# Optimization experiments

Hardware: AMD Instinct MI355X
Metric: run time of the kernel (lower is better)

The kernel has to match this reference:

```python
import jax, jax.numpy as jnp
import numpy as np

N, C, A, CI = 32768, 512, 64, 1024  # n_locations, content_size, address_size, controller_input_size
EPS = 1e-7


def setup_inputs() -> dict:
    key = jax.random.key(0)
    ks = jax.random.split(key, 12)
    g = lambda i, shape, s=1.0: jax.random.normal(ks[i], shape, dtype=jnp.float32) * s
    xav = lambda i, shape: g(i, shape, float(np.sqrt(2.0 / (shape[0] + shape[1]))))
    return {
        "controller_hidden_state": g(0, (N, 1)),
        "controller_input": g(1, (CI, 1)),
        "memory_contents": g(2, (N, C), 0.5),
        "memory_addresses": xav(3, (N, A)),
        "exp_mov_avg_similarity": g(4, (N, 1), 0.1),
        "W_query": xav(5, (C + A, N)),
        "b_query": jnp.zeros((C + A, 1), jnp.float32),
        "u_sharpen": xav(6, (1, N)),
        "b_sharpen": jnp.zeros((1,), jnp.float32),
        "u_lru": xav(7, (1, N)),
        "b_lru": jnp.zeros((1,), jnp.float32),
        "W_erase": xav(8, (C, N)),
        "b_erase": jnp.zeros((C, 1), jnp.float32),
        "W_content_hidden": xav(9, (C, N)),
        "W_content_input": xav(10, (C, CI)),
        "u_content_alpha": xav(11, (N + CI, 1)),
        "b_content_alpha": jnp.zeros((1, 1), jnp.float32),
    }


def reference(controller_hidden_state, controller_input, memory_contents, memory_addresses,
              exp_mov_avg_similarity, W_query, b_query, u_sharpen, b_sharpen, u_lru, b_lru,
              W_erase, b_erase, W_content_hidden, W_content_input, u_content_alpha,
              b_content_alpha):
    h, x = controller_hidden_state, controller_input
    # ---- address_memory ----
    full_mem = jnp.concatenate([memory_addresses, memory_contents], axis=1)  # [N, A+C]
    query = W_query @ h + b_query                                            # [A+C, 1]
    beta = jax.nn.softplus(u_sharpen @ h + b_sharpen) + 1.0                  # [1, 1]
    q = query[:, 0]
    q_norm = jnp.maximum(jnp.linalg.norm(q), EPS)
    m_norm = jnp.maximum(jnp.linalg.norm(full_mem, axis=1), EPS)             # [N]
    cos = (full_mem @ q) / (m_norm * q_norm)                                 # [N] cosine sim per location
    sim = (beta[0, 0] * cos)[:, None]                                        # [N, 1]
    gamma = jax.nn.sigmoid(u_lru @ h + b_lru)                                # [1, 1] LRU gate
    addr = jax.nn.softmax(sim - gamma * exp_mov_avg_similarity, axis=0)      # [N, 1]
    # (state buffer update, next-step only): new_ema = 0.1*ema + 0.9*sim
    # ---- update (vectorized erase/write over all N locations) ----
    erase = W_erase @ h + b_erase                                            # [C, 1]
    alpha = u_content_alpha.T @ jnp.concatenate([h, x], axis=0) + b_content_alpha  # [1, 1]
    cand = jax.nn.relu(W_content_hidden @ h + alpha * (W_content_input @ x))       # [C, 1]
    new_mem = (1.0 - addr * erase.T) * memory_contents + addr * cand.T       # [N, C]
    # ---- read (on updated memory) ----
    new_full = jnp.concatenate([memory_addresses, new_mem], axis=1)          # [N, A+C]
    read = new_full.T @ addr                                                 # [A+C, 1]
    return read
```

## Files before the change

kernel.cpp:

```cpp
#include <hip/hip_runtime.h>
#include <hip/hip_bf16.h>
#include <math.h>

#define NN 32768
#define CC 512
#define AA 64
#define CIN 1024
#define EPSV 1e-7f


#define QOFF 2128
#define SOFF 2704
#define PMOFF 35472
#define PAOFF 559760

__global__ __launch_bounds__(256) void k1_gemv(
    const float* __restrict__ h, const float* __restrict__ x,
    const float* __restrict__ Wq, const float* __restrict__ Wer,
    const float* __restrict__ Wch, const float* __restrict__ Wci,
    const float* __restrict__ ush, const float* __restrict__ ulr,
    const float* __restrict__ uca, float* __restrict__ ws)
{
    const int b = blockIdx.x, tid = threadIdx.x;
    const int wave = tid >> 6, lane = tid & 63;
    __shared__ float hs[4096];
    __shared__ float red[4][8];

    if (b < 1600) {
        const int rg = b >> 3, chunk = b & 7;
        const float4* h4 = reinterpret_cast<const float4*>(h) + chunk * 1024;
        float4* hs4 = reinterpret_cast<float4*>(hs);
        #pragma unroll
        for (int k = 0; k < 4; ++k) hs4[k * 256 + tid] = h4[k * 256 + tid];
        __syncthreads();
        const int r0 = rg * 8;
        const float* mat; int base;
        if (r0 < 576)       { mat = Wq;  base = 0; }
        else if (r0 < 1088) { mat = Wer; base = 576; }
        else                { mat = Wch; base = 1088; }
        const float4* m4 = reinterpret_cast<const float4*>(
            mat + (size_t)(r0 - base) * NN + chunk * 4096);
        const int rs = NN / 4;
        float acc[8] = {0,0,0,0,0,0,0,0};
        #pragma unroll
        for (int it = 0; it < 4; ++it) {
            float4 hb = hs4[it * 256 + tid];
            #pragma unroll
            for (int r = 0; r < 8; ++r) {
                float4 a = m4[(size_t)r * rs + it * 256 + tid];
                acc[r] += a.x * hb.x + a.y * hb.y + a.z * hb.z + a.w * hb.w;
            }
        }
        #pragma unroll
        for (int r = 0; r < 8; ++r) {
            #pragma unroll
            for (int off = 32; off >= 1; off >>= 1)
                acc[r] += __shfl_xor(acc[r], off);
        }
        if (lane == 0) {
            #pragma unroll
            for (int r = 0; r < 8; ++r) red[wave][r] = acc[r];
        }
        __syncthreads();
        if (tid < 8) {
            float v = red[0][tid] + red[1][tid] + red[2][tid] + red[3][tid];
            atomicAdd(ws + r0 + tid, v);
        }
    } else if (b < 1664) {
        const int rg = b - 1600;
        float4 xv = reinterpret_cast<const float4*>(x)[tid];
        const float4* m4 = reinterpret_cast<const float4*>(
            Wci + (size_t)rg * 8 * CIN);
        float acc[8];
        #pragma unroll
        for (int r = 0; r < 8; ++r) {
            float4 a = m4[r * 256 + tid];
            acc[r] = a.x * xv.x + a.y * xv.y + a.z * xv.z + a.w * xv.w;
        }
        #pragma unroll
        for (int r = 0; r < 8; ++r) {
            #pragma unroll
            for (int off = 32; off >= 1; off >>= 1)
                acc[r] += __shfl_xor(acc[r], off);
        }
        if (lane == 0) {
            #pragma unroll
            for (int r = 0; r < 8; ++r) red[wave][r] = acc[r];
        }
        __syncthreads();
        if (tid < 8) {
            float v = red[0][tid] + red[1][tid] + red[2][tid] + red[3][tid];
            ws[1600 + rg * 8 + tid] = v;
        }
    } else {
        const int t = b - 1664, sd = t >> 3, chunk = t & 7;
        const float* vec = (sd == 0) ? ush : (sd == 1) ? ulr : uca;
        const float4* v4 = reinterpret_cast<const float4*>(vec) + chunk * 1024;
        const float4* h4 = reinterpret_cast<const float4*>(h) + chunk * 1024;
        float acc = 0.f;
        #pragma unroll
        for (int it = 0; it < 4; ++it) {
            float4 a = v4[it * 256 + tid];
            float4 hb = h4[it * 256 + tid];
            acc += a.x * hb.x + a.y * hb.y + a.z * hb.z + a.w * hb.w;
        }
        if (sd == 2 && chunk == 0) {
            float4 a = reinterpret_cast<const float4*>(uca)[NN / 4 + tid];
            float4 xv = reinterpret_cast<const float4*>(x)[tid];
            acc += a.x * xv.x + a.y * xv.y + a.z * xv.z + a.w * xv.w;
        }
        #pragma unroll
        for (int off = 32; off >= 1; off >>= 1)
            acc += __shfl_xor(acc, off);
        if (lane == 0) red[wave][0] = acc;
        __syncthreads();
        if (tid == 0)
            atomicAdd(ws + 2112 + sd,
                      red[0][0] + red[1][0] + red[2][0] + red[3][0]);
    }
}

__global__ __launch_bounds__(256) void k1b_scalars(
    const float* __restrict__ bq, const float* __restrict__ bsh,
    const float* __restrict__ blr, const float* __restrict__ bca,
    float* __restrict__ ws)
{
    __shared__ float red[256];
    const int tid = threadIdx.x;
    float s = 0.f;
    for (int j = tid; j < 576; j += 256) {
        float q = ws[j] + bq[j];
        ws[QOFF + j] = q;
        s += q * q;
    }
    red[tid] = s; __syncthreads();
    for (int st = 128; st > 0; st >>= 1) {
        if (tid < st) red[tid] += red[tid + st];
        __syncthreads();
    }
    if (tid == 0) {
        float qn = fmaxf(sqrtf(red[0]), EPSV);
        float bp = ws[2112] + bsh[0];
        float beta = (bp > 20.f ? bp : log1pf(expf(bp))) + 1.0f;
        float gp = ws[2113] + blr[0];
        float gamma = 1.f / (1.f + expf(-gp));
        float alpha = ws[2114] + bca[0];
        ws[2112] = beta; ws[2113] = gamma; ws[2114] = alpha; ws[2115] = qn;
    }
}

__global__ __launch_bounds__(256) void k2_sim(
    const float* __restrict__ Mm, const float* __restrict__ Ad,
    const float* __restrict__ ema, const float* __restrict__ ws,
    float* __restrict__ ws_s)
{
    const int tid = threadIdx.x, wave = tid >> 6, lane = tid & 63;
    const float beta = ws[2112], gamma = ws[2113], qn = ws[2115];
    const float ql = ws[QOFF + lane];
    float4 qa = *reinterpret_cast<const float4*>(ws + QOFF + 64 + lane * 8);
    float4 qb = *reinterpret_cast<const float4*>(ws + QOFF + 68 + lane * 8);
    float qm[8] = {qa.x, qa.y, qa.z, qa.w, qb.x, qb.y, qb.z, qb.w};
    #pragma unroll
    for (int j = 0; j < 4; ++j) {
        const int i = blockIdx.x * 16 + wave * 4 + j;
        float a = Ad[(size_t)i * AA + lane];
        float4 m0 = *reinterpret_cast<const float4*>(Mm + (size_t)i * CC + lane * 8);
        float4 m1 = *reinterpret_cast<const float4*>(Mm + (size_t)i * CC + lane * 8 + 4);
        float mm[8] = {m0.x, m0.y, m0.z, m0.w, m1.x, m1.y, m1.z, m1.w};
        float dot = a * ql, nn = a * a;
        #pragma unroll
        for (int k = 0; k < 8; ++k) { float f = mm[k]; dot += f * qm[k]; nn += f * f; }
        #pragma unroll
        for (int off = 32; off >= 1; off >>= 1) {
            dot += __shfl_xor(dot, off);
            nn  += __shfl_xor(nn, off);
        }
        if (lane == 0) {
            float mn = fmaxf(sqrtf(nn), EPSV);
            ws_s[i] = beta * (dot / (mn * qn)) - gamma * ema[i];
        }
    }
}

__global__ __launch_bounds__(1024) void k3_softmax(float* __restrict__ ws)
{
    const float* s = ws + SOFF;
    __shared__ float lmx[16], lz[16], ls2[16], bc[1];
    const int tid = threadIdx.x, lane = tid & 63, wid = tid >> 6;
    float v[32];
    float mx = -1e30f;
    #pragma unroll
    for (int j = 0; j < 32; ++j) { v[j] = s[tid + 1024 * j]; mx = fmaxf(mx, v[j]); }
    #pragma unroll
    for (int off = 32; off >= 1; off >>= 1) mx = fmaxf(mx, __shfl_xor(mx, off));
    if (lane == 0) lmx[wid] = mx;
    __syncthreads();
    if (tid == 0) { float m = lmx[0]; for (int k = 1; k < 16; ++k) m = fmaxf(m, lmx[k]); bc[0] = m; }
    __syncthreads();
    mx = bc[0];
    float z = 0.f, s2 = 0.f;
    #pragma unroll
    for (int j = 0; j < 32; ++j) { float e = expf(v[j] - mx); z += e; s2 += e * e; }
    #pragma unroll
    for (int off = 32; off >= 1; off >>= 1) { z += __shfl_xor(z, off); s2 += __shfl_xor(s2, off); }
    if (lane == 0) { lz[wid] = z; ls2[wid] = s2; }
    __syncthreads();
    if (tid == 0) {
        float Z = 0.f, S = 0.f;
        for (int k = 0; k < 16; ++k) { Z += lz[k]; S += ls2[k]; }
        ws[2116] = mx; ws[2117] = 1.f / Z; ws[2118] = S / (Z * Z);
    }
}

__global__ __launch_bounds__(256) void k4_acc(
    const float* __restrict__ Mm, const float* __restrict__ Ad,
    const float* __restrict__ ws, float* __restrict__ pm, float* __restrict__ pa)
{
    __shared__ float lds[4][1024];
    const int b = blockIdx.x, tid = threadIdx.x, wave = tid >> 6, lane = tid & 63;
    const float* s = ws + SOFF;
    const float mx = ws[2116], invZ = ws[2117];
    if (b < 512) {
        float a1[8] = {0,0,0,0,0,0,0,0};
        float a2[8] = {0,0,0,0,0,0,0,0};
        for (int j = 0; j < 16; ++j) {
            const int i = b * 64 + j * 4 + wave;
            float w1 = expf(s[i] - mx) * invZ;
            float w2 = w1 * w1;
            float4 m0 = *reinterpret_cast<const float4*>(Mm + (size_t)i * CC + lane * 8);
            float4 m1 = *reinterpret_cast<const float4*>(Mm + (size_t)i * CC + lane * 8 + 4);
            float mm[8] = {m0.x, m0.y, m0.z, m0.w, m1.x, m1.y, m1.z, m1.w};
            #pragma unroll
            for (int k = 0; k < 8; ++k) { float f = mm[k]; a1[k] += w1 * f; a2[k] += w2 * f; }
        }
        #pragma unroll
        for (int k = 0; k < 8; ++k) {
            lds[wave][lane * 8 + k] = a1[k];
            lds[wave][512 + lane * 8 + k] = a2[k];
        }
        __syncthreads();
        for (int e = tid; e < 1024; e += 256) {
            float v = lds[0][e] + lds[1][e] + lds[2][e] + lds[3][e];
            pm[(size_t)e * 512 + b] = v;
        }
    } else {
        const int bb = b - 512;
        float acc = 0.f;
        for (int j = 0; j < 64; ++j) {
            const int i = bb * 256 + j * 4 + wave;
            float w1 = expf(s[i] - mx) * invZ;
            acc += w1 * Ad[(size_t)i * AA + lane];
        }
        lds[wave][lane] = acc;
        __syncthreads();
        if (tid < 64) {
            float v = lds[0][tid] + lds[1][tid] + lds[2][tid] + lds[3][tid];
            pa[tid * 128 + bb] = v;
        }
    }
}

__global__ __launch_bounds__(256) void k5_final(
    const float* __restrict__ ws, const float* __restrict__ pm,
    const float* __restrict__ pa, const float* __restrict__ ber,
    float* __restrict__ out)
{
    __shared__ float red[256];
    const int b = blockIdx.x, tid = threadIdx.x;
    if (b < 64) {
        float v = (tid < 128) ? pa[b * 128 + tid] : 0.f;
        red[tid] = v; __syncthreads();
        for (int st = 128; st > 0; st >>= 1) {
            if (tid < st) red[tid] += red[tid + st];
            __syncthreads();
        }
        if (tid == 0) out[b] = red[0];
    } else {
        const int c = b - 64;
        float v1 = pm[(size_t)c * 512 + tid] + pm[(size_t)c * 512 + tid + 256];
        float v2 = pm[(size_t)(512 + c) * 512 + tid] + pm[(size_t)(512 + c) * 512 + tid + 256];
        red[tid] = v1; __syncthreads();
        for (int st = 128; st > 0; st >>= 1) {
            if (tid < st) red[tid] += red[tid + st];
            __syncthreads();
        }
        float s1 = red[0];
        __syncthreads();
        red[tid] = v2; __syncthreads();
        for (int st = 128; st > 0; st >>= 1) {
            if (tid < st) red[tid] += red[tid + st];
            __syncthreads();
        }
        if (tid == 0) {
            float s2v = red[0];
            float er = ws[576 + c] + ber[c];
            float ch = ws[1088 + c], cx = ws[1600 + c];
            float alpha = ws[2114], S2 = ws[2118];
            float cand = fmaxf(ch + alpha * cx, 0.f);
            out[64 + c] = s1 - er * s2v + S2 * cand;
        }
    }
}

extern "C" void kernel_launch(void* const* d_in, const int* in_sizes, int n_in,
                              void* d_out, int out_size, void* d_ws, size_t ws_size,
                              hipStream_t stream)
{
    const float* h   = (const float*)d_in[0];
    const float* x   = (const float*)d_in[1];
    const float* Mm  = (const float*)d_in[2];
    const float* Ad  = (const float*)d_in[3];
    const float* ema = (const float*)d_in[4];
    const float* Wq  = (const float*)d_in[5];
    const float* bq  = (const float*)d_in[6];
    const float* ush = (const float*)d_in[7];
    const float* bsh = (const float*)d_in[8];
    const float* ulr = (const float*)d_in[9];
    const float* blr = (const float*)d_in[10];
    const float* Wer = (const float*)d_in[11];
    const float* ber = (const float*)d_in[12];
    const float* Wch = (const float*)d_in[13];
    const float* Wci = (const float*)d_in[14];
    const float* uca = (const float*)d_in[15];
    const float* bca = (const float*)d_in[16];

    float* ws   = (float*)d_ws;
    float* ws_s = ws + SOFF;
    float* pm   = ws + PMOFF;
    float* pa   = ws + PAOFF;
    float* out  = (float*)d_out;

    hipMemsetAsync(ws, 0, QOFF * sizeof(float), stream);

    hipLaunchKernelGGL(k1_gemv,    dim3(1688), dim3(256),  0, stream,
                       h, x, Wq, Wer, Wch, Wci, ush, ulr, uca, ws);
    hipLaunchKernelGGL(k1b_scalars, dim3(1),   dim3(256),  0, stream,
                       bq, bsh, blr, bca, ws);
    hipLaunchKernelGGL(k2_sim,     dim3(2048), dim3(256),  0, stream, Mm, Ad, ema, ws, ws_s);
    hipLaunchKernelGGL(k3_softmax, dim3(1),    dim3(1024), 0, stream, ws);
    hipLaunchKernelGGL(k4_acc,     dim3(640),  dim3(256),  0, stream, Mm, Ad, ws, pm, pa);
    hipLaunchKernelGGL(k5_final,   dim3(576),  dim3(256),  0, stream, ws, pm, pa, ber, out);
}
```

Baseline: 330.2 us.

## Fuse similarity, softmax and weighted accumulation into one pass with online softmax

Merges the similarity, global softmax and weighted-accumulation kernels into a single pass over memory using a per-wave online (running-max) softmax. Each block writes partial sums plus local max, Z and S2 statistics, and a small kernel rescales them into per-block coefficients that the final kernel applies. This removes the second full read of the 64 MB memory matrix and one launch. The GEMV weights are now loaded with nontemporal loads and software prefetch. The cost is extra exp and rescale work per row, fewer blocks in the fused kernel, and slightly different floating-point rounding.

```diff
diff --git a/kernel.cpp b/kernel.cpp
--- a/kernel.cpp
+++ b/kernel.cpp
@@ -10,9 +10,20 @@
 
 
 #define QOFF 2128
-#define SOFF 2704
-#define PMOFF 35472
-#define PAOFF 559760
+#define STOFF 2704
+#define SCOFF 4240
+#define PAOFF 5264
+#define PMOFF 38032
+
+typedef float floatx4 __attribute__((ext_vector_type(4)));
+
+__device__ __forceinline__ float4 ntload4(const float4* p) {
+    floatx4 v = __builtin_nontemporal_load(reinterpret_cast<const floatx4*>(p));
+    return make_float4(v.x, v.y, v.z, v.w);
+}
+__device__ __forceinline__ float ntloadf(const float* p) {
+    return __builtin_nontemporal_load(p);
+}
 
 __global__ __launch_bounds__(256) void k1_gemv(
     const float* __restrict__ h, const float* __restrict__ x,
@@ -42,13 +53,25 @@
             mat + (size_t)(r0 - base) * NN + chunk * 4096);
         const int rs = NN / 4;
         float acc[8] = {0,0,0,0,0,0,0,0};
+        float4 cur[8];
+        #pragma unroll
+        for (int r = 0; r < 8; ++r) cur[r] = ntload4(m4 + (size_t)r * rs + tid);
         #pragma unroll
         for (int it = 0; it < 4; ++it) {
+            float4 nxt[8];
+            if (it < 3) {
+                #pragma unroll
+                for (int r = 0; r < 8; ++r)
+                    nxt[r] = ntload4(m4 + (size_t)r * rs + (it + 1) * 256 + tid);
+            }
             float4 hb = hs4[it * 256 + tid];
             #pragma unroll
-            for (int r = 0; r < 8; ++r) {
-                float4 a = m4[(size_t)r * rs + it * 256 + tid];
-                acc[r] += a.x * hb.x + a.y * hb.y + a.z * hb.z + a.w * hb.w;
+            for (int r = 0; r < 8; ++r)
+                acc[r] += cur[r].x * hb.x + cur[r].y * hb.y +
+                          cur[r].z * hb.z + cur[r].w * hb.w;
+            if (it < 3) {
+                #pragma unroll
+                for (int r = 0; r < 8; ++r) cur[r] = nxt[r];
             }
         }
         #pragma unroll
@@ -74,7 +97,7 @@
         float acc[8];
         #pragma unroll
         for (int r = 0; r < 8; ++r) {
-            float4 a = m4[r * 256 + tid];
+            float4 a = ntload4(m4 + r * 256 + tid);
             acc[r] = a.x * xv.x + a.y * xv.y + a.z * xv.z + a.w * xv.w;
         }
         #pragma unroll
@@ -149,23 +172,28 @@
     }
 }
 
-__global__ __launch_bounds__(256) void k2_sim(
+__global__ __launch_bounds__(512) void k2f_fused(
     const float* __restrict__ Mm, const float* __restrict__ Ad,
     const float* __restrict__ ema, const float* __restrict__ ws,
-    float* __restrict__ ws_s)
-{
-    const int tid = threadIdx.x, wave = tid >> 6, lane = tid & 63;
+    float* __restrict__ pm, float* __restrict__ pa, float* __restrict__ stats)
+{
+    __shared__ float lw[8][1092];
+    const int b = blockIdx.x, tid = threadIdx.x, wave = tid >> 6, lane = tid & 63;
     const float beta = ws[2112], gamma = ws[2113], qn = ws[2115];
     const float ql = ws[QOFF + lane];
     float4 qa = *reinterpret_cast<const float4*>(ws + QOFF + 64 + lane * 8);
     float4 qb = *reinterpret_cast<const float4*>(ws + QOFF + 68 + lane * 8);
     float qm[8] = {qa.x, qa.y, qa.z, qa.w, qb.x, qb.y, qb.z, qb.w};
-    #pragma unroll
-    for (int j = 0; j < 4; ++j) {
-        const int i = blockIdx.x * 16 + wave * 4 + j;
-        float a = Ad[(size_t)i * AA + lane];
-        float4 m0 = *reinterpret_cast<const float4*>(Mm + (size_t)i * CC + lane * 8);
-        float4 m1 = *reinterpret_cast<const float4*>(Mm + (size_t)i * CC + lane * 8 + 4);
+
+    float a1[8] = {0,0,0,0,0,0,0,0};
+    float a2[8] = {0,0,0,0,0,0,0,0};
+    float aA = 0.f, m_run = -1e30f, Z = 0.f, S2 = 0.f;
+    const int base = b * 64 + wave * 8;
+    for (int j = 0; j < 8; ++j) {
+        const int i = base + j;
+        float a = ntloadf(Ad + (size_t)i * AA + lane);
+        float4 m0 = ntload4(reinterpret_cast<const float4*>(Mm + (size_t)i * CC + lane * 8));
+        float4 m1 = ntload4(reinterpret_cast<const float4*>(Mm + (size_t)i * CC + lane * 8 + 4));
         float mm[8] = {m0.x, m0.y, m0.z, m0.w, m1.x, m1.y, m1.z, m1.w};
         float dot = a * ql, nn = a * a;
         #pragma unroll
@@ -175,100 +203,105 @@
             dot += __shfl_xor(dot, off);
             nn  += __shfl_xor(nn, off);
         }
-        if (lane == 0) {
-            float mn = fmaxf(sqrtf(nn), EPSV);
-            ws_s[i] = beta * (dot / (mn * qn)) - gamma * ema[i];
-        }
-    }
-}
-
-__global__ __launch_bounds__(1024) void k3_softmax(float* __restrict__ ws)
-{
-    const float* s = ws + SOFF;
-    __shared__ float lmx[16], lz[16], ls2[16], bc[1];
-    const int tid = threadIdx.x, lane = tid & 63, wid = tid >> 6;
-    float v[32];
-    float mx = -1e30f;
+        float mn = fmaxf(sqrtf(nn), EPSV);
+        float s = beta * (dot / (mn * qn)) - gamma * ema[i];
+        if (s > m_run) {
+            float f = expf(m_run - s);
+            float f2 = f * f;
+            Z *= f; S2 *= f2; aA *= f;
+            #pragma unroll
+            for (int k = 0; k < 8; ++k) { a1[k] *= f; a2[k] *= f2; }
+            m_run = s;
+        }
+        float w = expf(s - m_run);
+        float w2 = w * w;
+        Z += w; S2 += w2; aA += w * a;
+        #pragma unroll
+        for (int k = 0; k < 8; ++k) { a1[k] += w * mm[k]; a2[k] += w2 * mm[k]; }
+    }
     #pragma unroll
-    for (int j = 0; j < 32; ++j) { v[j] = s[tid + 1024 * j]; mx = fmaxf(mx, v[j]); }
+    for (int k = 0; k < 8; ++k) {
+        lw[wave][lane * 8 + k] = a1[k];
+        lw[wave][512 + lane * 8 + k] = a2[k];
+    }
+    lw[wave][1024 + lane] = aA;
+    if (lane == 0) { lw[wave][1088] = m_run; lw[wave][1089] = Z; lw[wave][1090] = S2; }
+    __syncthreads();
+    float mb = lw[0][1088];
     #pragma unroll
-    for (int off = 32; off >= 1; off >>= 1) mx = fmaxf(mx, __shfl_xor(mx, off));
-    if (lane == 0) lmx[wid] = mx;
-    __syncthreads();
-    if (tid == 0) { float m = lmx[0]; for (int k = 1; k < 16; ++k) m = fmaxf(m, lmx[k]); bc[0] = m; }
-    __syncthreads();
-    mx = bc[0];
-    float z = 0.f, s2 = 0.f;
+    for (int w = 1; w < 8; ++w) mb = fmaxf(mb, lw[w][1088]);
+    float fw[8];
     #pragma unroll
-    for (int j = 0; j < 32; ++j) { float e = expf(v[j] - mx); z += e; s2 += e * e; }
-    #pragma unroll
-    for (int off = 32; off >= 1; off >>= 1) { z += __shfl_xor(z, off); s2 += __shfl_xor(s2, off); }
-    if (lane == 0) { lz[wid] = z; ls2[wid] = s2; }
-    __syncthreads();
+    for (int w = 0; w < 8; ++w) fw[w] = expf(lw[w][1088] - mb);
+    for (int e = tid; e < 1024; e += 512) {
+        float v = 0.f;
+        if (e < 512) {
+            #pragma unroll
+            for (int w = 0; w < 8; ++w) v += fw[w] * lw[w][e];
+        } else {
+            #pragma unroll
+            for (int w = 0; w < 8; ++w) v += fw[w] * fw[w] * lw[w][e];
+        }
+        pm[(size_t)e * 512 + b] = v;
+    }
+    if (tid < 64) {
+        float v = 0.f;
+        #pragma unroll
+        for (int w = 0; w < 8; ++w) v += fw[w] * lw[w][1024 + tid];
+        pa[tid * 512 + b] = v;
+    }
     if (tid == 0) {
-        float Z = 0.f, S = 0.f;
-        for (int k = 0; k < 16; ++k) { Z += lz[k]; S += ls2[k]; }
-        ws[2116] = mx; ws[2117] = 1.f / Z; ws[2118] = S / (Z * Z);
-    }
-}
-
-__global__ __launch_bounds__(256) void k4_acc(
-    const float* __restrict__ Mm, const float* __restrict__ Ad,
-    const float* __restrict__ ws, float* __restrict__ pm, float* __restrict__ pa)
-{
-    __shared__ float lds[4][1024];
-    const int b = blockIdx.x, tid = threadIdx.x, wave = tid >> 6, lane = tid & 63;
-    const float* s = ws + SOFF;
-    const float mx = ws[2116], invZ = ws[2117];
-    if (b < 512) {
-        float a1[8] = {0,0,0,0,0,0,0,0};
-        float a2[8] = {0,0,0,0,0,0,0,0};
-        for (int j = 0; j < 16; ++j) {
-            const int i = b * 64 + j * 4 + wave;
-            float w1 = expf(s[i] - mx) * invZ;
-            float w2 = w1 * w1;
-            float4 m0 = *reinterpret_cast<const float4*>(Mm + (size_t)i * CC + lane * 8);
-            float4 m1 = *reinterpret_cast<const float4*>(Mm + (size_t)i * CC + lane * 8 + 4);
-            float mm[8] = {m0.x, m0.y, m0.z, m0.w, m1.x, m1.y, m1.z, m1.w};
-            #pragma unroll
-            for (int k = 0; k < 8; ++k) { float f = mm[k]; a1[k] += w1 * f; a2[k] += w2 * f; }
-        }
-        #pragma unroll
-        for (int k = 0; k < 8; ++k) {
-            lds[wave][lane * 8 + k] = a1[k];
-            lds[wave][512 + lane * 8 + k] = a2[k];
-        }
-        __syncthreads();
-        for (int e = tid; e < 1024; e += 256) {
-            float v = lds[0][e] + lds[1][e] + lds[2][e] + lds[3][e];
-            pm[(size_t)e * 512 + b] = v;
-        }
-    } else {
-        const int bb = b - 512;
-        float acc = 0.f;
-        for (int j = 0; j < 64; ++j) {
-            const int i = bb * 256 + j * 4 + wave;
-            float w1 = expf(s[i] - mx) * invZ;
-            acc += w1 * Ad[(size_t)i * AA + lane];
-        }
-        lds[wave][lane] = acc;
-        __syncthreads();
-        if (tid < 64) {
-            float v = lds[0][tid] + lds[1][tid] + lds[2][tid] + lds[3][tid];
-            pa[tid * 128 + bb] = v;
-        }
-    }
+        float Zl = 0.f, S2l = 0.f;
+        #pragma unroll
+        for (int w = 0; w < 8; ++w) {
+            Zl  += fw[w] * lw[w][1089];
+            S2l += fw[w] * fw[w] * lw[w][1090];
+        }
+        stats[b] = mb; stats[512 + b] = Zl; stats[1024 + b] = S2l;
+    }
+}
+
+__global__ __launch_bounds__(512) void k3g(
+    const float* __restrict__ stats, float* __restrict__ sc,
+    float* __restrict__ ws)
+{
+    __shared__ float red[512];
+    const int t = threadIdx.x;
+    float m = stats[t];
+    red[t] = m; __syncthreads();
+    for (int st = 256; st > 0; st >>= 1) {
+        if (t < st) red[t] = fmaxf(red[t], red[t + st]);
+        __syncthreads();
+    }
+    float mx = red[0]; __syncthreads();
+    float e1 = expf(m - mx);
+    red[t] = e1 * stats[512 + t]; __syncthreads();
+    for (int st = 256; st > 0; st >>= 1) {
+        if (t < st) red[t] += red[t + st];
+        __syncthreads();
+    }
+    float Zg = red[0]; __syncthreads();
+    red[t] = e1 * e1 * stats[1024 + t]; __syncthreads();
+    for (int st = 256; st > 0; st >>= 1) {
+        if (t < st) red[t] += red[t + st];
+        __syncthreads();
+    }
+    float S2s = red[0];
+    float iZ = 1.f / Zg;
+    sc[t] = e1 * iZ;
+    sc[512 + t] = e1 * e1 * iZ * iZ;
+    if (t == 0) ws[2118] = S2s * iZ * iZ;
 }
 
 __global__ __launch_bounds__(256) void k5_final(
     const float* __restrict__ ws, const float* __restrict__ pm,
-    const float* __restrict__ pa, const float* __restrict__ ber,
-    float* __restrict__ out)
+    const float* __restrict__ pa, const float* __restrict__ sc,
+    const float* __restrict__ ber, float* __restrict__ out)
 {
     __shared__ float red[256];
     const int b = blockIdx.x, tid = threadIdx.x;
     if (b < 64) {
-        float v = (tid < 128) ? pa[b * 128 + tid] : 0.f;
+        float v = sc[tid] * pa[b * 512 + tid] + sc[tid + 256] * pa[b * 512 + tid + 256];
         red[tid] = v; __syncthreads();
         for (int st = 128; st > 0; st >>= 1) {
             if (tid < st) red[tid] += red[tid + st];
@@ -277,8 +310,10 @@
         if (tid == 0) out[b] = red[0];
     } else {
         const int c = b - 64;
-        float v1 = pm[(size_t)c * 512 + tid] + pm[(size_t)c * 512 + tid + 256];
-        float v2 = pm[(size_t)(512 + c) * 512 + tid] + pm[(size_t)(512 + c) * 512 + tid + 256];
+        float v1 = sc[tid] * pm[(size_t)c * 512 + tid]
+                 + sc[tid + 256] * pm[(size_t)c * 512 + tid + 256];
+        float v2 = sc[512 + tid] * pm[(size_t)(512 + c) * 512 + tid]
+                 + sc[512 + tid + 256] * pm[(size_t)(512 + c) * 512 + tid + 256];
         red[tid] = v1; __syncthreads();
         for (int st = 128; st > 0; st >>= 1) {
             if (tid < st) red[tid] += red[tid + st];
@@ -324,20 +359,22 @@
     const float* uca = (const float*)d_in[15];
     const float* bca = (const float*)d_in[16];
 
-    float* ws   = (float*)d_ws;
-    float* ws_s = ws + SOFF;
-    float* pm   = ws + PMOFF;
-    float* pa   = ws + PAOFF;
-    float* out  = (float*)d_out;
-
-    hipMemsetAsync(ws, 0, QOFF * sizeof(float), stream);
-
-    hipLaunchKernelGGL(k1_gemv,    dim3(1688), dim3(256),  0, stream,
+    float* ws    = (float*)d_ws;
+    float* stats = ws + STOFF;
+    float* sc    = ws + SCOFF;
+    float* pa    = ws + PAOFF;
+    float* pm    = ws + PMOFF;
+    float* out   = (float*)d_out;
+
+    (void)hipMemsetAsync(ws, 0, QOFF * sizeof(float), stream);
+
+    hipLaunchKernelGGL(k1_gemv,     dim3(1688), dim3(256), 0, stream,
                        h, x, Wq, Wer, Wch, Wci, ush, ulr, uca, ws);
-    hipLaunchKernelGGL(k1b_scalars, dim3(1),   dim3(256),  0, stream,
+    hipLaunchKernelGGL(k1b_scalars, dim3(1),    dim3(256), 0, stream,
                        bq, bsh, blr, bca, ws);
-    hipLaunchKernelGGL(k2_sim,     dim3(2048), dim3(256),  0, stream, Mm, Ad, ema, ws, ws_s);
-    hipLaunchKernelGGL(k3_softmax, dim3(1),    dim3(1024), 0, stream, ws);
-    hipLaunchKernelGGL(k4_acc,     dim3(640),  dim3(256),  0, stream, Mm, Ad, ws, pm, pa);
-    hipLaunchKernelGGL(k5_final,   dim3(576),  dim3(256),  0, stream, ws, pm, pa, ber, out);
-}
+    hipLaunchKernelGGL(k2f_fused,   dim3(512),  dim3(512), 0, stream,
+                       Mm, Ad, ema, ws, pm, pa, stats);
+    hipLaunchKernelGGL(k3g,         dim3(1),    dim3(512), 0, stream, stats, sc, ws);
+    hipLaunchKernelGGL(k5_final,    dim3(576),  dim3(256), 0, stream,
+                       ws, pm, pa, sc, ber, out);
+}
```

Result: faster. 281.0 us (-14.9%).
